# Kernel optimization log

Measured on AMD Instinct MI355X. Metric: run time of the kernel, lower is better.

## Reference

```python
import math
import jax, jax.numpy as jnp
import numpy as np

EPS = 1e-12
INV_4PI = 1.0 / (4.0 * math.pi)
B, NF = 32768, 3
RES_THETA, RES_PHI = 21, 41


def _make_quadrature(res_theta, res_phi):
    theta = np.linspace(0.0, math.pi, res_theta, dtype=np.float32)
    phi = np.linspace(0.0, 2.0 * math.pi, res_phi, dtype=np.float32)
    tm = 0.5 * (theta[:-1] + theta[1:])
    pm = 0.5 * (phi[:-1] + phi[1:])
    dth = theta[1:] - theta[:-1]
    dph = phi[1:] - phi[:-1]
    st, ct = np.sin(tm), np.cos(tm)
    sp, cp = np.sin(pm), np.cos(pm)
    vx = np.outer(st, cp).reshape(-1)
    vy = np.outer(st, sp).reshape(-1)
    vz = np.outer(ct, np.ones_like(pm)).reshape(-1)
    w = np.outer(st * dth, dph).reshape(-1)
    return (jnp.asarray(vx), jnp.asarray(vy), jnp.asarray(vz), jnp.asarray(w))


def setup_inputs() -> dict:
    key = jax.random.key(0)
    k1, k2, k3 = jax.random.split(key, 3)
    # positive densities O(1), flux magnitude <= 0.9*N (physically valid moments)
    dens = jax.random.uniform(k1, (B, 2, NF), minval=0.3, maxval=1.0, dtype=jnp.float32)
    fdir = jax.random.normal(k2, (B, 2, NF, 3), dtype=jnp.float32)
    fdir = fdir / jnp.clip(jnp.linalg.norm(fdir, axis=-1, keepdims=True), 1e-6)
    fmag = jax.random.uniform(k3, (B, 2, NF), minval=0.0, maxval=0.9, dtype=jnp.float32)
    F = fdir * (dens * fmag)[..., None]
    F4_in = jnp.concatenate([F, dens[..., None]], axis=-1)  # [B,2,NF,4]
    dir_x, dir_y, dir_z, quad_w = _make_quadrature(RES_THETA, RES_PHI)
    return {"F4_in": F4_in, "dir_x": dir_x, "dir_y": dir_y, "dir_z": dir_z, "quad_w": quad_w}


def _z_approxbis(f):
    f = jnp.clip(f, 0.0, 0.999999)
    f2 = f * f
    f4 = f2 * f2
    f6 = f4 * f2
    f8 = f4 * f4
    denom = 3.0 - 1.00651 * f2 - 0.962251 * f4 + 1.47353 * f6 - 0.48953 * f8
    p = 1.0 - 2.0 * (1.0 - f) * (1.0 + 1.01524 * f) / jnp.clip(denom, EPS)
    return 2.0 * f / jnp.clip(1.0 - p, 1e-06)


def _z_over_sinh_z(z):
    small = jnp.abs(z) < 1e-4
    zs = jnp.where(small, 1.0, z)  # avoid 0/0 in unused branch
    series = 1.0 - z * z / 6.0 + (z * z) * (z * z) / 120.0
    return jnp.where(small, series, zs / jnp.sinh(zs))


def _forward(F4_in, dir_x, dir_y, dir_z, quad_w):
    nf = F4_in.shape[2]
    N_e, N_ebar = F4_in[:, 0, 0, 3], F4_in[:, 1, 0, 3]
    F_e, F_ebar = F4_in[:, 0, 0, :3], F4_in[:, 1, 0, :3]
    if nf > 1:
        N_x = jnp.mean(F4_in[:, 0, 1:, 3], axis=1)
        N_xbar = jnp.mean(F4_in[:, 1, 1:, 3], axis=1)
        F_x = jnp.mean(F4_in[:, 0, 1:, :3], axis=1)
        F_xbar = jnp.mean(F4_in[:, 1, 1:, :3], axis=1)
    else:
        N_x, N_xbar, F_x, F_xbar = N_e, N_ebar, F_e, F_ebar
    N = jnp.clip(jnp.stack([N_e, N_ebar, N_x, N_xbar], axis=1), EPS)  # [B,4]
    F = jnp.stack([F_e, F_ebar, F_x, F_xbar], axis=1)  # [B,4,3]
    normF = jnp.sqrt(jnp.sum(F * F, axis=2))  # [B,4]
    fluxfac = jnp.clip(normF / N, 0.0, 0.999999)
    Z = _z_approxbis(fluxfac)  # [B,4]
    # mu: projection of unit direction onto flux direction, [B,4,D]
    mu = (F[:, :, 0, None] * dir_x + F[:, :, 1, None] * dir_y + F[:, :, 2, None] * dir_z) / jnp.clip(normF[..., None], EPS)
    g = N[..., None] * INV_4PI * _z_over_sinh_z(Z)[..., None] * jnp.exp(Z[..., None] * mu)  # [B,4,D]
    gnue, gnuebar, gnux, gnuxbar = g[:, 0], g[:, 1], g[:, 2], g[:, 3]
    delta = gnue - gnuebar - gnux + gnuxbar  # [B,D]
    Hpos = (delta >= 0.0).astype(g.dtype)
    Hneg = 1.0 - Hpos
    Iplus = jnp.sum(quad_w * jnp.maximum(delta, 0.0), axis=1)  # [B]
    Iminus = jnp.sum(quad_w * jnp.maximum(-delta, 0.0), axis=1)
    Ip_s = jnp.clip(Iplus, EPS)
    Im_s = jnp.clip(Iminus, EPS)
    third = jnp.full_like(Iplus, 1.0 / 3.0)
    coeff_pos = jnp.clip(jnp.where(Iplus < Iminus, third, 1.0 - 2.0 / 3.0 * (Im_s / Ip_s)), 0.0, 1.0)
    coeff_neg = jnp.clip(jnp.where(Iplus < Iminus, 1.0 - 2.0 / 3.0 * (Ip_s / Im_s), third), 0.0, 1.0)
    Psur = coeff_pos[:, None] * Hpos + coeff_neg[:, None] * Hneg  # [B,D]
    gnue_t = gnue * Psur + gnux * (1.0 - Psur)
    gnuebar_t = gnuebar * Psur + gnuxbar * (1.0 - Psur)
    gnux_t = 0.5 * (1.0 - Psur) * gnue + 0.5 * (1.0 + Psur) * gnux
    gnuxbar_t = 0.5 * (1.0 - Psur) * gnuebar + 0.5 * (1.0 + Psur) * gnuxbar
    g_t = jnp.stack([gnue_t, gnuebar_t, gnux_t, gnuxbar_t], axis=1)  # [B,4,D]
    gw = g_t * quad_w  # [B,4,D]
    newN = jnp.sum(gw, axis=2)  # [B,4]
    newF = jnp.stack([jnp.sum(gw * dir_x, axis=2), jnp.sum(gw * dir_y, axis=2), jnp.sum(gw * dir_z, axis=2)], axis=2)  # [B,4,3]
    b = F4_in.shape[0]
    if nf > 1:
        F_nu = jnp.concatenate([newF[:, 0:1], jnp.broadcast_to(newF[:, 2:3], (b, nf - 1, 3))], axis=1)
        F_nubar = jnp.concatenate([newF[:, 1:2], jnp.broadcast_to(newF[:, 3:4], (b, nf - 1, 3))], axis=1)
        N_nu = jnp.concatenate([newN[:, 0:1], jnp.broadcast_to(newN[:, 2:3], (b, nf - 1))], axis=1)
        N_nubar = jnp.concatenate([newN[:, 1:2], jnp.broadcast_to(newN[:, 3:4], (b, nf - 1))], axis=1)
    else:
        F_nu, F_nubar = newF[:, 0:1], newF[:, 1:2]
        N_nu, N_nubar = newN[:, 0:1], newN[:, 1:2]
    nu = jnp.concatenate([F_nu, N_nu[..., None]], axis=-1)  # [B,NF,4]
    nubar = jnp.concatenate([F_nubar, N_nubar[..., None]], axis=-1)
    F4mix = jnp.stack([nu, nubar], axis=1)  # [B,2,NF,4]
    growth = jnp.sqrt(jnp.clip(Iplus * Iminus, 0.0))
    return (F4mix, growth)


def reference(F4_in, dir_x, dir_y, dir_z, quad_w):
    return _forward(F4_in, dir_x, dir_y, dir_z, quad_w)
```

## Files before the change

kernel.cpp:

```cpp
#include <hip/hip_runtime.h>
#include <math.h>

#define EPSF     1e-12f
#define INV_4PI  0.07957747154594767f
#define LOG2E    1.4426950408889634f

typedef float v2f __attribute__((ext_vector_type(2)));

#if __has_builtin(__builtin_elementwise_fma)
#define FMA2(a, b, c) __builtin_elementwise_fma((a), (b), (c))
#else
#define FMA2(a, b, c) ((a) * (b) + (c))
#endif

#define EXP2(x) __builtin_amdgcn_exp2f(x)

__device__ __forceinline__ v2f bcast(float x) { v2f r; r.x = x; r.y = x; return r; }

__device__ __forceinline__ float zapprox(float f) {
    float f2 = f * f;
    float f4 = f2 * f2;
    float f6 = f4 * f2;
    float f8 = f4 * f4;
    float denom = 3.0f - 1.00651f * f2 - 0.962251f * f4 + 1.47353f * f6 - 0.48953f * f8;
    denom = fmaxf(denom, EPSF);
    float p = 1.0f - 2.0f * (1.0f - f) * (1.0f + 1.01524f * f) / denom;
    return 2.0f * f / fmaxf(1.0f - p, 1e-6f);
}

__device__ __forceinline__ float z_over_sinh(float z) {
    float zz = z * z;
    float series = 1.0f - zz / 6.0f + zz * zz / 120.0f;
    float E = __expf(z);
    float s = 0.5f * (E - 1.0f / E);
    float r = z / s;
    return (z < 1e-4f) ? series : r;
}

__device__ __forceinline__ float4 setup_spec(float N, float Fx, float Fy, float Fz) {
    N = fmaxf(N, EPSF);
    float nf = sqrtf(Fx * Fx + Fy * Fy + Fz * Fz);
    float f  = fminf(fmaxf(nf / N, 0.0f), 0.999999f);
    float Z  = zapprox(f);
    float A  = N * INV_4PI * z_over_sinh(Z);
    float sc = Z * LOG2E / fmaxf(nf, EPSF);
    return make_float4(Fx * sc, Fy * sc, Fz * sc, log2f(A));
}

__global__ __launch_bounds__(256) void spec_kernel(
    const float* __restrict__ F4, float4* __restrict__ ws, int B)
{
    int t = blockIdx.x * blockDim.x + threadIdx.x;
    if (t >= 4 * B) return;
    int b = t >> 2, s = t & 3;
    const float4* row = (const float4*)(F4 + (size_t)b * 24);
    float N, Fx, Fy, Fz;
    if (s == 0) {
        float4 a = row[0];  N = a.w; Fx = a.x; Fy = a.y; Fz = a.z;
    } else if (s == 1) {
        float4 a = row[3];  N = a.w; Fx = a.x; Fy = a.y; Fz = a.z;
    } else if (s == 2) {
        float4 a = row[1], c = row[2];
        N = 0.5f * (a.w + c.w); Fx = 0.5f * (a.x + c.x);
        Fy = 0.5f * (a.y + c.y); Fz = 0.5f * (a.z + c.z);
    } else {
        float4 a = row[4], c = row[5];
        N = 0.5f * (a.w + c.w); Fx = 0.5f * (a.x + c.x);
        Fy = 0.5f * (a.y + c.y); Fz = 0.5f * (a.z + c.z);
    }
    ws[(size_t)b * 4 + s] = setup_spec(N, Fx, Fy, Fz);
}

__device__ __forceinline__ void add4(float4& a, const float4 b) {
    a.x += b.x; a.y += b.y; a.z += b.z; a.w += b.w;
}

__global__ __launch_bounds__(1024, 8) void box3d_kernel(
    const float4* __restrict__ ws,
    const float* __restrict__ dxp, const float* __restrict__ dyp,
    const float* __restrict__ dzp, const float* __restrict__ qwp,
    float* __restrict__ out, int B, int ndir)
{
    __shared__ float4 red[16][64][3];

    const int lane = threadIdx.x & 63;
    const int w    = __builtin_amdgcn_readfirstlane(threadIdx.x >> 6);
    const int b    = blockIdx.x * 64 + lane;
    const bool live = (b < B);

    v2f zx01, zy01, zz01, la01, zx23, zy23, zz23, la23;
    if (live) {
        const float4* wsb = ws + (size_t)b * 4;
        float4 s0 = wsb[0], s1 = wsb[1], s2 = wsb[2], s3 = wsb[3];
        zx01.x = s0.x; zx01.y = s1.x;  zx23.x = s2.x; zx23.y = s3.x;
        zy01.x = s0.y; zy01.y = s1.y;  zy23.x = s2.y; zy23.y = s3.y;
        zz01.x = s0.z; zz01.y = s1.z;  zz23.x = s2.z; zz23.y = s3.z;
        la01.x = s0.w; la01.y = s1.w;  la23.x = s2.w; la23.y = s3.w;
    } else {
        zx01 = zy01 = zz01 = la01 = bcast(0.0f);
        zx23 = zy23 = zz23 = la23 = bcast(0.0f);
    }
    const v2f two = bcast(2.0f);

    const int nst   = ndir >> 1;
    const int chunk = (nst + 15) >> 4;
    const int d0    = w * chunk;
    const int d1    = (d0 + chunk < nst) ? d0 + chunk : nst;

    const v2f zero = bcast(0.0f);
    v2f auv0 = zero, auv1 = zero, auv2 = zero, auv3 = zero;
    v2f asv0 = zero, asv1 = zero, asv2 = zero, asv3 = zero;
    v2f ag0  = zero, ag1  = zero, ag2  = zero, ag3  = zero;

    int dd = (d0 < d1) ? d0 : 0;
    float qx = dxp[dd], qy = dyp[dd], qz = dzp[dd], qw = qwp[dd];

    #pragma clang loop unroll(disable)
    for (int d = d0; d < d1; ++d) {
        int dn = (d + 1 < d1) ? d + 1 : d;
        float nqx = dxp[dn], nqy = dyp[dn], nqz = dzp[dn], nqw = qwp[dn];

        v2f t01 = FMA2(zx01, bcast(qx), FMA2(zy01, bcast(qy), FMA2(zz01, bcast(qz), la01)));
        v2f t23 = FMA2(zx23, bcast(qx), FMA2(zy23, bcast(qy), FMA2(zz23, bcast(qz), la23)));

        {
            v2f g01, g23;
            g01.x = EXP2(t01.x); g01.y = EXP2(t01.y);
            g23.x = EXP2(t23.x); g23.y = EXP2(t23.y);
            v2f uv = bcast(qw) * (g01 - g23);
            v2f wg = bcast(qw) * g23;
            bool c = (uv.x >= uv.y);
            v2f suv; suv.x = c ? uv.x : 0.0f; suv.y = c ? uv.y : 0.0f;
            auv0 += uv;  auv1 = FMA2(uv, bcast(qx), auv1);
            auv2 = FMA2(uv, bcast(qy), auv2);  auv3 = FMA2(uv, bcast(qz), auv3);
            asv0 += suv; asv1 = FMA2(suv, bcast(qx), asv1);
            asv2 = FMA2(suv, bcast(qy), asv2); asv3 = FMA2(suv, bcast(qz), asv3);
            ag0  += wg;  ag1  = FMA2(wg, bcast(qx), ag1);
            ag2  = FMA2(wg, bcast(qy), ag2);   ag3  = FMA2(wg, bcast(qz), ag3);
        }
        {
            v2f n01 = FMA2(two, la01, -t01);
            v2f n23 = FMA2(two, la23, -t23);
            v2f g01, g23;
            g01.x = EXP2(n01.x); g01.y = EXP2(n01.y);
            g23.x = EXP2(n23.x); g23.y = EXP2(n23.y);
            v2f uv = bcast(qw) * (g01 - g23);
            v2f wg = bcast(qw) * g23;
            bool c = (uv.x >= uv.y);
            v2f suv; suv.x = c ? uv.x : 0.0f; suv.y = c ? uv.y : 0.0f;
            auv0 += uv;  auv1 = FMA2(uv, bcast(-qx), auv1);
            auv2 = FMA2(uv, bcast(-qy), auv2);  auv3 = FMA2(uv, bcast(-qz), auv3);
            asv0 += suv; asv1 = FMA2(suv, bcast(-qx), asv1);
            asv2 = FMA2(suv, bcast(-qy), asv2); asv3 = FMA2(suv, bcast(-qz), asv3);
            ag0  += wg;  ag1  = FMA2(wg, bcast(-qx), ag1);
            ag2  = FMA2(wg, bcast(-qy), ag2);   ag3  = FMA2(wg, bcast(-qz), ag3);
        }
        qx = nqx; qy = nqy; qz = nqz; qw = nqw;
    }

    float4 rA0 = make_float4(auv0.x, auv0.y, auv1.x, auv1.y);
    float4 rA1 = make_float4(auv2.x, auv2.y, auv3.x, auv3.y);
    float4 rA2 = make_float4(asv0.x, asv0.y, asv1.x, asv1.y);
    float4 rB0 = make_float4(asv2.x, asv2.y, asv3.x, asv3.y);
    float4 rB1 = make_float4(ag0.x,  ag0.y,  ag1.x,  ag1.y);
    float4 rB2 = make_float4(ag2.x,  ag2.y,  ag3.x,  ag3.y);

    red[w][lane][0] = rA0; red[w][lane][1] = rA1; red[w][lane][2] = rA2;
    __syncthreads();
    if (w < 4) {
        #pragma unroll
        for (int o = 4; o < 16; o += 4) {
            add4(rA0, red[w + o][lane][0]);
            add4(rA1, red[w + o][lane][1]);
            add4(rA2, red[w + o][lane][2]);
        }
        red[w][lane][0] = rA0; red[w][lane][1] = rA1; red[w][lane][2] = rA2;
    }
    __syncthreads();
    if (w == 0) {
        #pragma unroll
        for (int o = 1; o < 4; ++o) {
            add4(rA0, red[o][lane][0]);
            add4(rA1, red[o][lane][1]);
            add4(rA2, red[o][lane][2]);
        }
    }
    __syncthreads();
    red[w][lane][0] = rB0; red[w][lane][1] = rB1; red[w][lane][2] = rB2;
    __syncthreads();
    if (w < 4) {
        #pragma unroll
        for (int o = 4; o < 16; o += 4) {
            add4(rB0, red[w + o][lane][0]);
            add4(rB1, red[w + o][lane][1]);
            add4(rB2, red[w + o][lane][2]);
        }
        red[w][lane][0] = rB0; red[w][lane][1] = rB1; red[w][lane][2] = rB2;
    }
    __syncthreads();
    if (w != 0 || !live) return;
    #pragma unroll
    for (int o = 1; o < 4; ++o) {
        add4(rB0, red[o][lane][0]);
        add4(rB1, red[o][lane][1]);
        add4(rB2, red[o][lane][2]);
    }

    float ut0 = rA0.x, vt0 = rA0.y, ut1 = rA0.z, vt1 = rA0.w;
    float ut2 = rA1.x, vt2 = rA1.y, ut3 = rA1.z, vt3 = rA1.w;
    float up0 = rA2.x, vp0 = rA2.y, up1 = rA2.z, vp1 = rA2.w;
    float up2 = rB0.x, vp2 = rB0.y, up3 = rB0.z, vp3 = rB0.w;
    float gx0 = rB1.x, gy0 = rB1.y, gx1 = rB1.z, gy1 = rB1.w;
    float gx2 = rB2.x, gy2 = rB2.y, gx3 = rB2.z, gy3 = rB2.w;

    float ip = fmaxf(up0 - vp0, 0.0f);
    float im = fmaxf(ip - ut0 + vt0, 0.0f);

    float Ips = fmaxf(ip, EPSF), Ims = fmaxf(im, EPSF);
    const float third = 1.0f / 3.0f;
    float cp, cn;
    if (ip < im) {
        cp = third;
        cn = fminf(fmaxf(1.0f - (2.0f / 3.0f) * (Ips / Ims), 0.0f), 1.0f);
    } else {
        cp = fminf(fmaxf(1.0f - (2.0f / 3.0f) * (Ims / Ips), 0.0f), 1.0f);
        cn = third;
    }

    float P0 = cp * up0 + cn * (ut0 - up0), Q0 = cp * vp0 + cn * (vt0 - vp0);
    float P1 = cp * up1 + cn * (ut1 - up1), Q1 = cp * vp1 + cn * (vt1 - vp1);
    float P2 = cp * up2 + cn * (ut2 - up2), Q2 = cp * vp2 + cn * (vt2 - vp2);
    float P3 = cp * up3 + cn * (ut3 - up3), Q3 = cp * vp3 + cn * (vt3 - vp3);

    float4* o4 = (float4*)out + (size_t)b * 6;
    float4 oe = make_float4(gx1 + P1, gx2 + P2, gx3 + P3, gx0 + P0);
    float4 ox = make_float4(gx1 + 0.5f * (ut1 - P1), gx2 + 0.5f * (ut2 - P2),
                            gx3 + 0.5f * (ut3 - P3), gx0 + 0.5f * (ut0 - P0));
    float4 ob = make_float4(gy1 + Q1, gy2 + Q2, gy3 + Q3, gy0 + Q0);
    float4 oxb = make_float4(gy1 + 0.5f * (vt1 - Q1), gy2 + 0.5f * (vt2 - Q2),
                             gy3 + 0.5f * (vt3 - Q3), gy0 + 0.5f * (vt0 - Q0));
    o4[0] = oe;  o4[1] = ox;  o4[2] = ox;
    o4[3] = ob;  o4[4] = oxb; o4[5] = oxb;
    out[(size_t)B * 24 + b] = sqrtf(fmaxf(ip * im, 0.0f));
}

extern "C" void kernel_launch(void* const* d_in, const int* in_sizes, int n_in,
                              void* d_out, int out_size, void* d_ws, size_t ws_size,
                              hipStream_t stream) {
    const float* F4 = (const float*)d_in[0];
    const float* dx = (const float*)d_in[1];
    const float* dy = (const float*)d_in[2];
    const float* dz = (const float*)d_in[3];
    const float* qw = (const float*)d_in[4];
    float* out = (float*)d_out;

    int B = in_sizes[0] / 24;
    int ndir = in_sizes[1];
    float4* ws = (float4*)d_ws;

    int t1 = 4 * B;
    spec_kernel<<<(t1 + 255) / 256, 256, 0, stream>>>(F4, ws, B);
    int blocks = (B + 63) / 64;
    box3d_kernel<<<blocks, 1024, 0, stream>>>(ws, dx, dy, dz, qw, out, B, ndir);
}
```

Measured before the change: 92.06 us.

## Fuse spectrum setup into main kernel and software-pipeline exp2 over directions

Removes the separate spec_kernel launch: the first 256 threads of each block compute the four per-sample spectrum parameters into shared memory, and all waves then read them after a barrier. The direction loop is restructured so the exp2 evaluations for the next direction are issued before accumulating the previous one, with unroll 2 in place of the explicit prefetch. This saves one launch and the workspace round trip through global memory, and gives more overlap of transcendental work with the FMAs. In exchange it adds a block barrier plus serialized setup work done by only a quarter of the threads, and an extra sync before the reduction reuses shared memory.

```diff
diff --git a/kernel.cpp b/kernel.cpp
--- a/kernel.cpp
+++ b/kernel.cpp
@@ -47,59 +47,56 @@
     return make_float4(Fx * sc, Fy * sc, Fz * sc, log2f(A));
 }
 
-__global__ __launch_bounds__(256) void spec_kernel(
-    const float* __restrict__ F4, float4* __restrict__ ws, int B)
-{
-    int t = blockIdx.x * blockDim.x + threadIdx.x;
-    if (t >= 4 * B) return;
-    int b = t >> 2, s = t & 3;
-    const float4* row = (const float4*)(F4 + (size_t)b * 24);
-    float N, Fx, Fy, Fz;
-    if (s == 0) {
-        float4 a = row[0];  N = a.w; Fx = a.x; Fy = a.y; Fz = a.z;
-    } else if (s == 1) {
-        float4 a = row[3];  N = a.w; Fx = a.x; Fy = a.y; Fz = a.z;
-    } else if (s == 2) {
-        float4 a = row[1], c = row[2];
-        N = 0.5f * (a.w + c.w); Fx = 0.5f * (a.x + c.x);
-        Fy = 0.5f * (a.y + c.y); Fz = 0.5f * (a.z + c.z);
-    } else {
-        float4 a = row[4], c = row[5];
-        N = 0.5f * (a.w + c.w); Fx = 0.5f * (a.x + c.x);
-        Fy = 0.5f * (a.y + c.y); Fz = 0.5f * (a.z + c.z);
-    }
-    ws[(size_t)b * 4 + s] = setup_spec(N, Fx, Fy, Fz);
-}
-
 __device__ __forceinline__ void add4(float4& a, const float4 b) {
     a.x += b.x; a.y += b.y; a.z += b.z; a.w += b.w;
 }
 
 __global__ __launch_bounds__(1024, 8) void box3d_kernel(
-    const float4* __restrict__ ws,
+    const float* __restrict__ F4,
     const float* __restrict__ dxp, const float* __restrict__ dyp,
     const float* __restrict__ dzp, const float* __restrict__ qwp,
     float* __restrict__ out, int B, int ndir)
 {
+    __shared__ float4 sh_spec[4][64];
     __shared__ float4 red[16][64][3];
 
-    const int lane = threadIdx.x & 63;
-    const int w    = __builtin_amdgcn_readfirstlane(threadIdx.x >> 6);
-    const int b    = blockIdx.x * 64 + lane;
-    const bool live = (b < B);
-
+    const int tid  = threadIdx.x;
+    const int lane = tid & 63;
+    const int w    = __builtin_amdgcn_readfirstlane(tid >> 6);
+    const int base = blockIdx.x * 64;
+    const int b    = base + lane;
+
+    if (tid < 256) {
+        int bl = tid & 63, s = tid >> 6;
+        int bb = base + bl;
+        float N = 1.0f, Fx = 0.0f, Fy = 0.0f, Fz = 0.0f;
+        if (bb < B) {
+            const float4* row = (const float4*)(F4 + (size_t)bb * 24);
+            if (s == 0) {
+                float4 a = row[0];  N = a.w; Fx = a.x; Fy = a.y; Fz = a.z;
+            } else if (s == 1) {
+                float4 a = row[3];  N = a.w; Fx = a.x; Fy = a.y; Fz = a.z;
+            } else if (s == 2) {
+                float4 a = row[1], c = row[2];
+                N = 0.5f * (a.w + c.w); Fx = 0.5f * (a.x + c.x);
+                Fy = 0.5f * (a.y + c.y); Fz = 0.5f * (a.z + c.z);
+            } else {
+                float4 a = row[4], c = row[5];
+                N = 0.5f * (a.w + c.w); Fx = 0.5f * (a.x + c.x);
+                Fy = 0.5f * (a.y + c.y); Fz = 0.5f * (a.z + c.z);
+            }
+        }
+        sh_spec[s][bl] = setup_spec(N, Fx, Fy, Fz);
+    }
+    __syncthreads();
+
+    float4 f0 = sh_spec[0][lane], f1 = sh_spec[1][lane];
+    float4 f2 = sh_spec[2][lane], f3 = sh_spec[3][lane];
     v2f zx01, zy01, zz01, la01, zx23, zy23, zz23, la23;
-    if (live) {
-        const float4* wsb = ws + (size_t)b * 4;
-        float4 s0 = wsb[0], s1 = wsb[1], s2 = wsb[2], s3 = wsb[3];
-        zx01.x = s0.x; zx01.y = s1.x;  zx23.x = s2.x; zx23.y = s3.x;
-        zy01.x = s0.y; zy01.y = s1.y;  zy23.x = s2.y; zy23.y = s3.y;
-        zz01.x = s0.z; zz01.y = s1.z;  zz23.x = s2.z; zz23.y = s3.z;
-        la01.x = s0.w; la01.y = s1.w;  la23.x = s2.w; la23.y = s3.w;
-    } else {
-        zx01 = zy01 = zz01 = la01 = bcast(0.0f);
-        zx23 = zy23 = zz23 = la23 = bcast(0.0f);
-    }
+    zx01.x = f0.x; zx01.y = f1.x;  zx23.x = f2.x; zx23.y = f3.x;
+    zy01.x = f0.y; zy01.y = f1.y;  zy23.x = f2.y; zy23.y = f3.y;
+    zz01.x = f0.z; zz01.y = f1.z;  zz23.x = f2.z; zz23.y = f3.z;
+    la01.x = f0.w; la01.y = f1.w;  la23.x = f2.w; la23.y = f3.w;
     const v2f two = bcast(2.0f);
 
     const int nst   = ndir >> 1;
@@ -112,51 +109,65 @@
     v2f asv0 = zero, asv1 = zero, asv2 = zero, asv3 = zero;
     v2f ag0  = zero, ag1  = zero, ag2  = zero, ag3  = zero;
 
-    int dd = (d0 < d1) ? d0 : 0;
-    float qx = dxp[dd], qy = dyp[dd], qz = dzp[dd], qw = qwp[dd];
-
-    #pragma clang loop unroll(disable)
-    for (int d = d0; d < d1; ++d) {
-        int dn = (d + 1 < d1) ? d + 1 : d;
-        float nqx = dxp[dn], nqy = dyp[dn], nqz = dzp[dn], nqw = qwp[dn];
-
+    v2f Pg01, Pg23, Ng01, Ng23;
+    float pqx, pqy, pqz, pqw;
+    {
+        int dd = (d0 < d1) ? d0 : 0;
+        pqx = dxp[dd]; pqy = dyp[dd]; pqz = dzp[dd]; pqw = qwp[dd];
+        v2f t01 = FMA2(zx01, bcast(pqx), FMA2(zy01, bcast(pqy), FMA2(zz01, bcast(pqz), la01)));
+        v2f t23 = FMA2(zx23, bcast(pqx), FMA2(zy23, bcast(pqy), FMA2(zz23, bcast(pqz), la23)));
+        v2f n01 = FMA2(two, la01, -t01);
+        v2f n23 = FMA2(two, la23, -t23);
+        Pg01.x = EXP2(t01.x); Pg01.y = EXP2(t01.y);
+        Pg23.x = EXP2(t23.x); Pg23.y = EXP2(t23.y);
+        Ng01.x = EXP2(n01.x); Ng01.y = EXP2(n01.y);
+        Ng23.x = EXP2(n23.x); Ng23.y = EXP2(n23.y);
+    }
+
+#define ACCUM_UNIT(G01P, G23P, G01N, G23N, QX, QY, QZ, QW)                         \
+    {                                                                              \
+        v2f uvP = ((G01P) - (G23P)) * bcast(QW);                                   \
+        v2f wgP = bcast(QW) * (G23P);                                              \
+        bool cP = (uvP.x >= uvP.y);                                                \
+        v2f suvP; suvP.x = cP ? uvP.x : 0.0f; suvP.y = cP ? uvP.y : 0.0f;          \
+        auv0 += uvP;  auv1 = FMA2(uvP, bcast(QX), auv1);                           \
+        auv2 = FMA2(uvP, bcast(QY), auv2);  auv3 = FMA2(uvP, bcast(QZ), auv3);     \
+        asv0 += suvP; asv1 = FMA2(suvP, bcast(QX), asv1);                          \
+        asv2 = FMA2(suvP, bcast(QY), asv2); asv3 = FMA2(suvP, bcast(QZ), asv3);    \
+        ag0  += wgP;  ag1  = FMA2(wgP, bcast(QX), ag1);                            \
+        ag2  = FMA2(wgP, bcast(QY), ag2);   ag3  = FMA2(wgP, bcast(QZ), ag3);      \
+        v2f uvN = ((G01N) - (G23N)) * bcast(QW);                                   \
+        v2f wgN = bcast(QW) * (G23N);                                              \
+        bool cN = (uvN.x >= uvN.y);                                                \
+        v2f suvN; suvN.x = cN ? uvN.x : 0.0f; suvN.y = cN ? uvN.y : 0.0f;          \
+        auv0 += uvN;  auv1 = FMA2(uvN, bcast(-(QX)), auv1);                        \
+        auv2 = FMA2(uvN, bcast(-(QY)), auv2);  auv3 = FMA2(uvN, bcast(-(QZ)), auv3);\
+        asv0 += suvN; asv1 = FMA2(suvN, bcast(-(QX)), asv1);                       \
+        asv2 = FMA2(suvN, bcast(-(QY)), asv2); asv3 = FMA2(suvN, bcast(-(QZ)), asv3);\
+        ag0  += wgN;  ag1  = FMA2(wgN, bcast(-(QX)), ag1);                         \
+        ag2  = FMA2(wgN, bcast(-(QY)), ag2);   ag3  = FMA2(wgN, bcast(-(QZ)), ag3);\
+    }
+
+    #pragma unroll 2
+    for (int d = d0 + 1; d < d1; ++d) {
+        float qx = dxp[d], qy = dyp[d], qz = dzp[d], qw = qwp[d];
         v2f t01 = FMA2(zx01, bcast(qx), FMA2(zy01, bcast(qy), FMA2(zz01, bcast(qz), la01)));
         v2f t23 = FMA2(zx23, bcast(qx), FMA2(zy23, bcast(qy), FMA2(zz23, bcast(qz), la23)));
-
-        {
-            v2f g01, g23;
-            g01.x = EXP2(t01.x); g01.y = EXP2(t01.y);
-            g23.x = EXP2(t23.x); g23.y = EXP2(t23.y);
-            v2f uv = bcast(qw) * (g01 - g23);
-            v2f wg = bcast(qw) * g23;
-            bool c = (uv.x >= uv.y);
-            v2f suv; suv.x = c ? uv.x : 0.0f; suv.y = c ? uv.y : 0.0f;
-            auv0 += uv;  auv1 = FMA2(uv, bcast(qx), auv1);
-            auv2 = FMA2(uv, bcast(qy), auv2);  auv3 = FMA2(uv, bcast(qz), auv3);
-            asv0 += suv; asv1 = FMA2(suv, bcast(qx), asv1);
-            asv2 = FMA2(suv, bcast(qy), asv2); asv3 = FMA2(suv, bcast(qz), asv3);
-            ag0  += wg;  ag1  = FMA2(wg, bcast(qx), ag1);
-            ag2  = FMA2(wg, bcast(qy), ag2);   ag3  = FMA2(wg, bcast(qz), ag3);
-        }
-        {
-            v2f n01 = FMA2(two, la01, -t01);
-            v2f n23 = FMA2(two, la23, -t23);
-            v2f g01, g23;
-            g01.x = EXP2(n01.x); g01.y = EXP2(n01.y);
-            g23.x = EXP2(n23.x); g23.y = EXP2(n23.y);
-            v2f uv = bcast(qw) * (g01 - g23);
-            v2f wg = bcast(qw) * g23;
-            bool c = (uv.x >= uv.y);
-            v2f suv; suv.x = c ? uv.x : 0.0f; suv.y = c ? uv.y : 0.0f;
-            auv0 += uv;  auv1 = FMA2(uv, bcast(-qx), auv1);
-            auv2 = FMA2(uv, bcast(-qy), auv2);  auv3 = FMA2(uv, bcast(-qz), auv3);
-            asv0 += suv; asv1 = FMA2(suv, bcast(-qx), asv1);
-            asv2 = FMA2(suv, bcast(-qy), asv2); asv3 = FMA2(suv, bcast(-qz), asv3);
-            ag0  += wg;  ag1  = FMA2(wg, bcast(-qx), ag1);
-            ag2  = FMA2(wg, bcast(-qy), ag2);   ag3  = FMA2(wg, bcast(-qz), ag3);
-        }
-        qx = nqx; qy = nqy; qz = nqz; qw = nqw;
-    }
+        v2f n01 = FMA2(two, la01, -t01);
+        v2f n23 = FMA2(two, la23, -t23);
+        v2f Cg01, Cg23, Cn01, Cn23;
+        Cg01.x = EXP2(t01.x); Cg01.y = EXP2(t01.y);
+        Cg23.x = EXP2(t23.x); Cg23.y = EXP2(t23.y);
+        Cn01.x = EXP2(n01.x); Cn01.y = EXP2(n01.y);
+        Cn23.x = EXP2(n23.x); Cn23.y = EXP2(n23.y);
+
+        ACCUM_UNIT(Pg01, Pg23, Ng01, Ng23, pqx, pqy, pqz, pqw);
+
+        Pg01 = Cg01; Pg23 = Cg23; Ng01 = Cn01; Ng23 = Cn23;
+        pqx = qx; pqy = qy; pqz = qz; pqw = qw;
+    }
+    ACCUM_UNIT(Pg01, Pg23, Ng01, Ng23, pqx, pqy, pqz, pqw);
+#undef ACCUM_UNIT
 
     float4 rA0 = make_float4(auv0.x, auv0.y, auv1.x, auv1.y);
     float4 rA1 = make_float4(auv2.x, auv2.y, auv3.x, auv3.y);
@@ -165,6 +176,7 @@
     float4 rB1 = make_float4(ag0.x,  ag0.y,  ag1.x,  ag1.y);
     float4 rB2 = make_float4(ag2.x,  ag2.y,  ag3.x,  ag3.y);
 
+    __syncthreads();
     red[w][lane][0] = rA0; red[w][lane][1] = rA1; red[w][lane][2] = rA2;
     __syncthreads();
     if (w < 4) {
@@ -198,7 +210,7 @@
         red[w][lane][0] = rB0; red[w][lane][1] = rB1; red[w][lane][2] = rB2;
     }
     __syncthreads();
-    if (w != 0 || !live) return;
+    if (w != 0 || b >= B) return;
     #pragma unroll
     for (int o = 1; o < 4; ++o) {
         add4(rB0, red[o][lane][0]);
@@ -256,10 +268,8 @@
 
     int B = in_sizes[0] / 24;
     int ndir = in_sizes[1];
-    float4* ws = (float4*)d_ws;
-
-    int t1 = 4 * B;
-    spec_kernel<<<(t1 + 255) / 256, 256, 0, stream>>>(F4, ws, B);
+    (void)d_ws; (void)ws_size;
+
     int blocks = (B + 63) / 64;
-    box3d_kernel<<<blocks, 1024, 0, stream>>>(ws, dx, dy, dz, qw, out, B, ndir);
-}
+    box3d_kernel<<<blocks, 1024, 0, stream>>>(F4, dx, dy, dz, qw, out, B, ndir);
+}
```

Result: faster. 87.98 us (-4.4%).
